# Optimization experiments

Measured on AMD Instinct MI355X. Metric: run time of the kernel, lower is better.

Reference implementation:

```python
import jax, jax.numpy as jnp
import numpy as np

N_BUS = 2048


def setup_inputs() -> dict:
    key = jax.random.key(0)
    ks = jax.random.split(key, 16)
    n_x, n_rbf, n_bus, batch = 4096, 1024, N_BUS, 8192
    s = lambda fan_in: 1.0 / np.sqrt(fan_in)
    return {
        "x": jax.random.normal(ks[0], (batch, n_x), dtype=jnp.float32),
        "W_h": jax.random.uniform(ks[1], (n_rbf, n_x), jnp.float32, -s(n_x), s(n_x)),
        "b_h": jax.random.uniform(ks[2], (n_rbf,), jnp.float32, -s(n_x), s(n_x)),
        "W_h2": jax.random.uniform(ks[3], (n_rbf, n_rbf), jnp.float32, -s(n_rbf), s(n_rbf)),
        "b_h2": jax.random.uniform(ks[4], (n_rbf,), jnp.float32, -s(n_rbf), s(n_rbf)),
        "W_y": jax.random.uniform(ks[5], (2 * n_bus, n_rbf), jnp.float32, -s(n_rbf), s(n_rbf)),
        "b_y": jax.random.uniform(ks[6], (2 * n_bus,), jnp.float32, -s(n_rbf), s(n_rbf)),
        "G": jax.random.uniform(ks[7], (n_bus, n_bus), dtype=jnp.float32),
        "Bm": jax.random.uniform(ks[8], (n_bus, n_bus), dtype=jnp.float32),
        "bias_p": jnp.zeros((1, n_bus), jnp.float32),
        "bias_q": jnp.zeros((1, n_bus), jnp.float32),
        "W_p": jax.random.uniform(ks[9], (n_bus, n_bus), jnp.float32, -s(n_bus), s(n_bus)),
        "b_p": jax.random.uniform(ks[10], (n_bus,), jnp.float32, -s(n_bus), s(n_bus)),
        "W_q": jax.random.uniform(ks[11], (n_bus, n_bus), jnp.float32, -s(n_bus), s(n_bus)),
        "b_q": jax.random.uniform(ks[12], (n_bus,), jnp.float32, -s(n_bus), s(n_bus)),
    }


def reference(x, W_h, b_h, W_h2, b_h2, W_y, b_y, G, Bm, bias_p, bias_q, W_p, b_p, W_q, b_q):
    n_bus = N_BUS
    # encoder (intended math: ReLU activations)
    h1 = jax.nn.relu(x @ W_h.T + b_h)
    h2 = jax.nn.relu(h1 @ W_h2.T + b_h2)
    uw = h2 @ W_y.T + b_y                     # [B, 2*n_bus]
    u, w = uw[:, :n_bus], uw[:, n_bus:]
    # decoder: algebraically identical to summing the masked outer products over dim 2:
    # p_i = sum_k (u_i u_k + w_i w_k) G_ik + (w_i u_k - u_i w_k) B_ik
    #     = u_i (G u)_i + w_i (G w)_i + w_i (B u)_i - u_i (B w)_i
    Gu = u @ G.T
    Gw = w @ G.T
    Bu = u @ Bm.T
    Bw = w @ Bm.T
    p = u * Gu + w * Gw + w * Bu - u * Bw + bias_p
    q = w * Gu - u * Gw - u * Bu - w * Bw + bias_q
    p = p @ W_p.T + b_p
    q = q @ W_q.T + b_q
    return (uw, p, q)
```

## Files before the change

### kernel.cpp

```cpp
#include <hip/hip_runtime.h>
#include <stdint.h>

typedef __bf16 bf16;
typedef __bf16 bf16x8 __attribute__((ext_vector_type(8)));
typedef __bf16 bf16x4 __attribute__((ext_vector_type(4)));
typedef float  f32x4  __attribute__((ext_vector_type(4)));

__device__ __forceinline__ void async_load16(const void* g, void* l) {
    __builtin_amdgcn_global_load_lds(
        (const __attribute__((address_space(1))) void*)g,
        (__attribute__((address_space(3))) void*)l,
        16, 0, 0);
}

__global__ __launch_bounds__(256) void cast_f32_bf16(
        const float* __restrict__ s, bf16* __restrict__ d, int n) {
    int i = (blockIdx.x * 256 + threadIdx.x) * 8;
    if (i >= n) return;
    f32x4 v0 = *(const f32x4*)(s + i);
    f32x4 v1 = *(const f32x4*)(s + i + 4);
    bf16x8 o;
    o[0] = (bf16)v0[0]; o[1] = (bf16)v0[1]; o[2] = (bf16)v0[2]; o[3] = (bf16)v0[3];
    o[4] = (bf16)v1[0]; o[5] = (bf16)v1[1]; o[6] = (bf16)v1[2]; o[7] = (bf16)v1[3];
    *(bf16x8*)(d + i) = o;
}

__global__ __launch_bounds__(256) void fill_f32(float* p, float v, int n) {
    int i = blockIdx.x * 256 + threadIdx.x;
    if (i < n) p[i] = v;
}

template<int RELU, int WF32, int WBF16>
__global__ __launch_bounds__(256, 3) void gemm_bt(
        const bf16* __restrict__ A, int lda,
        const bf16* __restrict__ B, int ldb,
        const float* __restrict__ bias,
        float* __restrict__ Cf, int ldcf,
        bf16* __restrict__ Cb, int ldcb,
        int M, int N, int K) {
    (void)M; (void)N;
    __shared__ __attribute__((aligned(16))) bf16 lA[128 * 32];
    __shared__ __attribute__((aligned(16))) bf16 lB[128 * 32];

    const int t = threadIdx.x;
    const int w = t >> 6, lane = t & 63;
    const int wm = w >> 1, wn = w & 1;
    const int m0 = blockIdx.y * 128, n0 = blockIdx.x * 128;
    const int lane15 = lane & 15, quad = lane >> 4;

    f32x4 acc[4][4] = {};

    const int srow = lane >> 2;
    const int scol = (lane & 3) * 8;
    const int c0 = 2 * w, c1 = 2 * w + 1;
    const bf16* gA0 = A + (size_t)(m0 + c0 * 16 + srow) * lda + scol;
    const bf16* gA1 = A + (size_t)(m0 + c1 * 16 + srow) * lda + scol;
    const bf16* gB0 = B + (size_t)(n0 + c0 * 16 + srow) * ldb + scol;
    const bf16* gB1 = B + (size_t)(n0 + c1 * 16 + srow) * ldb + scol;
    bf16* lA0 = &lA[c0 * 512];
    bf16* lA1 = &lA[c1 * 512];
    bf16* lB0 = &lB[c0 * 512];
    bf16* lB1 = &lB[c1 * 512];

    const bf16* fA = &lA[(wm * 64 + lane15) * 32 + quad * 8];
    const bf16* fB = &lB[(wn * 64 + lane15) * 32 + quad * 8];

    for (int k0 = 0; k0 < K; k0 += 32) {
        async_load16(gA0, lA0);
        async_load16(gA1, lA1);
        async_load16(gB0, lB0);
        async_load16(gB1, lB1);
        gA0 += 32; gA1 += 32; gB0 += 32; gB1 += 32;
        __syncthreads();
        bf16x8 a[4], b[4];
#pragma unroll
        for (int i = 0; i < 4; i++) a[i] = *(const bf16x8*)(fA + i * 16 * 32);
#pragma unroll
        for (int j = 0; j < 4; j++) b[j] = *(const bf16x8*)(fB + j * 16 * 32);
#pragma unroll
        for (int i = 0; i < 4; i++)
#pragma unroll
            for (int j = 0; j < 4; j++)
                acc[i][j] = __builtin_amdgcn_mfma_f32_16x16x32_bf16(a[i], b[j], acc[i][j], 0, 0, 0);
        __syncthreads();
    }

#pragma unroll
    for (int i = 0; i < 4; i++) {
        int row = m0 + wm * 64 + i * 16 + quad * 4;
#pragma unroll
        for (int j = 0; j < 4; j++) {
            int col = n0 + wn * 64 + j * 16 + lane15;
            float bv = bias ? bias[col] : 0.0f;
#pragma unroll
            for (int r = 0; r < 4; r++) {
                float v = acc[i][j][r] + bv;
                if (RELU) v = v > 0.0f ? v : 0.0f;
                if (WF32)  Cf[(size_t)(row + r) * ldcf + col] = v;
                if (WBF16) Cb[(size_t)(row + r) * ldcb + col] = (bf16)v;
            }
        }
    }
}

template<int RELU, int WF32, int WBF16>
__global__ __launch_bounds__(512, 2) void gemm256(
        const bf16* __restrict__ A, int lda,
        const bf16* __restrict__ B, int ldb,
        const float* __restrict__ bias,
        float* __restrict__ Cf, int ldcf,
        bf16* __restrict__ Cb, int ldcb,
        int K) {
    __shared__ __attribute__((aligned(128))) char sm[131072];

    const int t = threadIdx.x;
    const int w = t >> 6;
    const int lane = t & 63;
    const int wm = w >> 2, wn = w & 3;
    const int l15 = lane & 15, quad = lane >> 4;

    const int gx = gridDim.x;
    const int nwg = gx * gridDim.y;
    const int orig = blockIdx.y * gx + blockIdx.x;
    const int cpx = nwg >> 3;
    const int wg = (orig & 7) * cpx + (orig >> 3);
    const int m0 = (wg / gx) << 8;
    const int n0 = (wg % gx) << 8;

    f32x4 acc[8][4] = {};

    const int srow = t >> 3;
    const int scol = ((t & 7) ^ (srow & 7)) << 3;
    const bf16* gA = A + (size_t)(m0 + srow) * lda + scol;
    const bf16* gB = B + (size_t)(n0 + srow) * ldb + scol;
    char* smA = sm + w * 1024;
    char* smB = sm + 65536 + w * 1024;
    const size_t rstepA = (size_t)lda << 6;
    const size_t rstepB = (size_t)ldb << 6;

    const int swz = (quad ^ (l15 & 7)) << 4;
    const char* aRd0 = sm + ((wm * 128 + l15) << 7) + swz;
    const char* bRd0 = sm + 65536 + ((wn * 64 + l15) << 7) + swz;
    const char* aRd1 = (const char*)((uintptr_t)aRd0 ^ 64);
    const char* bRd1 = (const char*)((uintptr_t)bRd0 ^ 64);

    bf16x8 a[4][2], b[4][2];
    unsigned boff = 0;

#define STG_A(c, nb) async_load16(gA + (c) * rstepA, smA + (nb) + (c) * 8192)
#define STG_B(c, nb) async_load16(gB + (c) * rstepB, smB + (nb) + (c) * 8192)
#define RD_A(Mq) do { _Pragma("unroll") \
    for (int i = 0; i < 4; i++) { \
        a[i][0] = *(const bf16x8*)(aRd0 + boff + (Mq) * 8192 + i * 2048); \
        a[i][1] = *(const bf16x8*)(aRd1 + boff + (Mq) * 8192 + i * 2048); } } while (0)
#define RD_B(Nq) do { _Pragma("unroll") \
    for (int j = 0; j < 2; j++) { \
        b[(Nq) * 2 + j][0] = *(const bf16x8*)(bRd0 + boff + ((Nq) * 2 + j) * 2048); \
        b[(Nq) * 2 + j][1] = *(const bf16x8*)(bRd1 + boff + ((Nq) * 2 + j) * 2048); } } while (0)
#define MMA(Mq, Nq) do { _Pragma("unroll") \
    for (int i = 0; i < 4; i++) { _Pragma("unroll") \
        for (int j = 0; j < 2; j++) { \
            acc[(Mq) * 4 + i][(Nq) * 2 + j] = __builtin_amdgcn_mfma_f32_16x16x32_bf16( \
                a[i][0], b[(Nq) * 2 + j][0], acc[(Mq) * 4 + i][(Nq) * 2 + j], 0, 0, 0); \
            acc[(Mq) * 4 + i][(Nq) * 2 + j] = __builtin_amdgcn_mfma_f32_16x16x32_bf16( \
                a[i][1], b[(Nq) * 2 + j][1], acc[(Mq) * 4 + i][(Nq) * 2 + j], 0, 0, 0); } } } while (0)
#define BARP() do { __builtin_amdgcn_s_barrier(); \
    __builtin_amdgcn_sched_barrier(0); } while (0)
#define WAITVM(N) do { \
    asm volatile("s_waitcnt vmcnt(" #N ")" ::: "memory"); } while (0)

    STG_B(0, 0); STG_B(1, 0); STG_B(2, 0); STG_B(3, 0);
    STG_A(0, 0); STG_A(2, 0); STG_A(1, 0); STG_A(3, 0);
    gA += 64; gB += 64;
    WAITVM(0);
    BARP();

    const int nt = K >> 6;
#define KTILE(PF) do { \
    const unsigned nboff = boff ^ 32768u; \
     \
    RD_A(0); RD_B(0); RD_B(1); \
    if (PF) { STG_B(0, nboff); STG_B(1, nboff); STG_B(2, nboff); STG_B(3, nboff); } \
    MMA(0, 0); MMA(0, 1); \
    if (PF) { WAITVM(4); } \
    BARP(); \
     \
    RD_A(1); \
    if (PF) { STG_A(0, nboff); STG_A(2, nboff); STG_A(1, nboff); STG_A(3, nboff); } \
    MMA(1, 0); MMA(1, 1); \
    if (PF) { WAITVM(2); gA += 64; gB += 64; } \
    BARP(); \
    boff = nboff; \
} while (0)

    for (int T = 0; T < nt - 1; ++T) KTILE(1);
    KTILE(0);
#undef KTILE
#undef STG_A
#undef STG_B
#undef RD_A
#undef RD_B
#undef MMA
#undef BARP
#undef WAITVM

#pragma unroll
    for (int i = 0; i < 8; i++) {
        int row = m0 + wm * 128 + i * 16 + quad * 4;
#pragma unroll
        for (int j = 0; j < 4; j++) {
            int col = n0 + wn * 64 + j * 16 + l15;
            float bv = bias ? bias[col] : 0.0f;
#pragma unroll
            for (int r = 0; r < 4; r++) {
                float v = acc[i][j][r] + bv;
                if (RELU) v = v > 0.0f ? v : 0.0f;
                if (WF32)  Cf[(size_t)(row + r) * ldcf + col] = v;
                if (WBF16) Cb[(size_t)(row + r) * ldcb + col] = (bf16)v;
            }
        }
    }
}

__global__ __launch_bounds__(256) void combine_pq(
        const bf16* __restrict__ uwb,
        const bf16* __restrict__ GBu, const bf16* __restrict__ GBw,
        const float* __restrict__ bias_p, const float* __restrict__ bias_q,
        bf16* __restrict__ pp, bf16* __restrict__ qp) {
    int idx = (blockIdx.x * 256 + threadIdx.x) * 4;
    int row = idx >> 11;
    int col = idx & 2047;
    size_t base = (size_t)row * 4096 + col;
    bf16x4 u4  = *(const bf16x4*)(uwb + base);
    bf16x4 w4  = *(const bf16x4*)(uwb + base + 2048);
    bf16x4 gu4 = *(const bf16x4*)(GBu + base);
    bf16x4 bu4 = *(const bf16x4*)(GBu + base + 2048);
    bf16x4 gw4 = *(const bf16x4*)(GBw + base);
    bf16x4 bw4 = *(const bf16x4*)(GBw + base + 2048);
    bf16x4 po, qo;
#pragma unroll
    for (int r = 0; r < 4; r++) {
        float u = (float)u4[r], w = (float)w4[r];
        float gu = (float)gu4[r], gw = (float)gw4[r];
        float bu = (float)bu4[r], bw = (float)bw4[r];
        float p = u * gu + w * gw + w * bu - u * bw + bias_p[col + r];
        float q = w * gu - u * gw - u * bu - w * bw + bias_q[col + r];
        po[r] = (bf16)p;
        qo[r] = (bf16)q;
    }
    *(bf16x4*)(pp + idx) = po;
    *(bf16x4*)(qp + idx) = qo;
}

extern "C" void kernel_launch(void* const* d_in, const int* in_sizes, int n_in,
                              void* d_out, int out_size, void* d_ws, size_t ws_size,
                              hipStream_t stream) {
    (void)in_sizes; (void)n_in;
    const int BT = 8192, NX = 4096, NR = 1024, NB = 2048;

    const float* x      = (const float*)d_in[0];
    const float* W_h    = (const float*)d_in[1];
    const float* b_h    = (const float*)d_in[2];
    const float* W_h2   = (const float*)d_in[3];
    const float* b_h2   = (const float*)d_in[4];
    const float* W_y    = (const float*)d_in[5];
    const float* b_y    = (const float*)d_in[6];
    const float* G      = (const float*)d_in[7];
    const float* Bm     = (const float*)d_in[8];
    const float* bias_p = (const float*)d_in[9];
    const float* bias_q = (const float*)d_in[10];
    const float* W_p    = (const float*)d_in[11];
    const float* b_p    = (const float*)d_in[12];
    const float* W_q    = (const float*)d_in[13];
    const float* b_q    = (const float*)d_in[14];
    float* out = (float*)d_out;

    const size_t NEED = 320864256ull;
    if (ws_size < NEED) {
        fill_f32<<<dim3((out_size + 255) / 256), dim3(256), 0, stream>>>(
            out, (float)(ws_size >> 20), out_size);
        return;
    }
    char* ws = (char*)d_ws;
    bf16* xb   = (bf16*)(ws + 0);
    bf16* GBu  = (bf16*)(ws + 0);
    bf16* uwb  = (bf16*)(ws + 67108864);
    bf16* GBw  = (bf16*)(ws + 134217728);
    bf16* h1   = (bf16*)(ws + 201326592);
    bf16* pp   = (bf16*)(ws + 201326592);
    bf16* h2   = (bf16*)(ws + 218103808);
    bf16* qp   = (bf16*)(ws + 234881024);
    bf16* whb  = (bf16*)(ws + 268435456);
    bf16* wh2b = (bf16*)(ws + 276824064);
    bf16* wyb  = (bf16*)(ws + 278921216);
    bf16* gbm  = (bf16*)(ws + 287309824);
    bf16* wpb  = (bf16*)(ws + 304087040);
    bf16* wqb  = (bf16*)(ws + 312475648);

    dim3 blk(256);
    auto cast = [&](const float* s, bf16* d, int n) {
        cast_f32_bf16<<<dim3((n / 8 + 255) / 256), blk, 0, stream>>>(s, d, n);
    };
    cast(x,    xb,   BT * NX);
    cast(W_h,  whb,  NR * NX);
    cast(W_h2, wh2b, NR * NR);
    cast(W_y,  wyb,  NX * NR);
    cast(G,    gbm,            NB * NB);
    cast(Bm,   gbm + (size_t)NB * NB, NB * NB);
    cast(W_p,  wpb,  NB * NB);
    cast(W_q,  wqb,  NB * NB);

    gemm_bt<1, 0, 1><<<dim3(NR / 128, BT / 128), blk, 0, stream>>>(
        xb, NX, whb, NX, b_h, nullptr, 0, h1, NR, BT, NR, NX);
    gemm_bt<1, 0, 1><<<dim3(NR / 128, BT / 128), blk, 0, stream>>>(
        h1, NR, wh2b, NR, b_h2, nullptr, 0, h2, NR, BT, NR, NR);

    gemm256<0, 1, 1><<<dim3(NX / 256, BT / 256), dim3(512), 0, stream>>>(
        h2, NR, wyb, NR, b_y, out, NX, uwb, NX, NR);
    gemm256<0, 0, 1><<<dim3(NX / 256, BT / 256), dim3(512), 0, stream>>>(
        uwb,      NX, gbm, NB, nullptr, nullptr, 0, GBu, NX, NB);
    gemm256<0, 0, 1><<<dim3(NX / 256, BT / 256), dim3(512), 0, stream>>>(
        uwb + NB, NX, gbm, NB, nullptr, nullptr, 0, GBw, NX, NB);
    combine_pq<<<dim3(BT * NB / 4 / 256), blk, 0, stream>>>(
        uwb, GBu, GBw, bias_p, bias_q, pp, qp);
    gemm256<0, 1, 0><<<dim3(NB / 256, BT / 256), dim3(512), 0, stream>>>(
        pp, NB, wpb, NB, b_p, out + (size_t)BT * NX, NB, nullptr, 0, NB);
    gemm256<0, 1, 0><<<dim3(NB / 256, BT / 256), dim3(512), 0, stream>>>(
        qp, NB, wqb, NB, b_q, out + (size_t)BT * NX + (size_t)BT * NB, NB, nullptr, 0, NB);
}
```

Baseline: 1.277 ms.

## Restructure gemm256 K-loop into finer-grained staged prefetch with setprio and remapped wave tiles

The gemm256 main loop is split into three barrier phases, each issuing part of the next tile's global-to-LDS loads between MFMA groups, with half of the next-next tile prefetched early. MFMA blocks are wrapped in s_setprio to favour math waves. The warp-to-subtile mapping changes so that each wave covers interleaved 64-row and 32-column sub-blocks, with the epilogue indexing adjusted to match. One of the decoder GEMMs is also switched to the 128-tile gemm_bt kernel. The goal is to hide load latency better, at the cost of more barriers and harder-to-verify wait counts.

```diff
diff --git a/kernel.cpp b/kernel.cpp
--- a/kernel.cpp
+++ b/kernel.cpp
@@ -139,62 +139,73 @@
     const size_t rstepB = (size_t)ldb << 6;
 
     const int swz = (quad ^ (l15 & 7)) << 4;
-    const char* aRd0 = sm + ((wm * 128 + l15) << 7) + swz;
-    const char* bRd0 = sm + 65536 + ((wn * 64 + l15) << 7) + swz;
+    const char* aRd0 = sm + (wm << 13) + (l15 << 7) + swz;
+    const char* bRd0 = sm + 65536 + ((wn >> 1) << 13) + ((((wn & 1) << 5) + l15) << 7) + swz;
     const char* aRd1 = (const char*)((uintptr_t)aRd0 ^ 64);
     const char* bRd1 = (const char*)((uintptr_t)bRd0 ^ 64);
 
     bf16x8 a[4][2], b[4][2];
     unsigned boff = 0;
 
-#define STG_A(c, nb) async_load16(gA + (c) * rstepA, smA + (nb) + (c) * 8192)
-#define STG_B(c, nb) async_load16(gB + (c) * rstepB, smB + (nb) + (c) * 8192)
+#define STG_A(c, ko, nb) async_load16(gA + (ko) + (c) * rstepA, smA + (nb) + (c) * 8192)
+#define STG_B(c, ko, nb) async_load16(gB + (ko) + (c) * rstepB, smB + (nb) + (c) * 8192)
 #define RD_A(Mq) do { _Pragma("unroll") \
     for (int i = 0; i < 4; i++) { \
-        a[i][0] = *(const bf16x8*)(aRd0 + boff + (Mq) * 8192 + i * 2048); \
-        a[i][1] = *(const bf16x8*)(aRd1 + boff + (Mq) * 8192 + i * 2048); } } while (0)
+        a[i][0] = *(const bf16x8*)(aRd0 + boff + (Mq) * 16384 + i * 2048); \
+        a[i][1] = *(const bf16x8*)(aRd1 + boff + (Mq) * 16384 + i * 2048); } } while (0)
 #define RD_B(Nq) do { _Pragma("unroll") \
     for (int j = 0; j < 2; j++) { \
-        b[(Nq) * 2 + j][0] = *(const bf16x8*)(bRd0 + boff + ((Nq) * 2 + j) * 2048); \
-        b[(Nq) * 2 + j][1] = *(const bf16x8*)(bRd1 + boff + ((Nq) * 2 + j) * 2048); } } while (0)
-#define MMA(Mq, Nq) do { _Pragma("unroll") \
+        b[(Nq) * 2 + j][0] = *(const bf16x8*)(bRd0 + boff + (Nq) * 16384 + j * 2048); \
+        b[(Nq) * 2 + j][1] = *(const bf16x8*)(bRd1 + boff + (Nq) * 16384 + j * 2048); } } while (0)
+#define MMA(Mq, Nq) do { __builtin_amdgcn_s_setprio(1); _Pragma("unroll") \
     for (int i = 0; i < 4; i++) { _Pragma("unroll") \
         for (int j = 0; j < 2; j++) { \
             acc[(Mq) * 4 + i][(Nq) * 2 + j] = __builtin_amdgcn_mfma_f32_16x16x32_bf16( \
                 a[i][0], b[(Nq) * 2 + j][0], acc[(Mq) * 4 + i][(Nq) * 2 + j], 0, 0, 0); \
             acc[(Mq) * 4 + i][(Nq) * 2 + j] = __builtin_amdgcn_mfma_f32_16x16x32_bf16( \
-                a[i][1], b[(Nq) * 2 + j][1], acc[(Mq) * 4 + i][(Nq) * 2 + j], 0, 0, 0); } } } while (0)
+                a[i][1], b[(Nq) * 2 + j][1], acc[(Mq) * 4 + i][(Nq) * 2 + j], 0, 0, 0); } } \
+    __builtin_amdgcn_s_setprio(0); } while (0)
 #define BARP() do { __builtin_amdgcn_s_barrier(); \
     __builtin_amdgcn_sched_barrier(0); } while (0)
-#define WAITVM(N) do { \
-    asm volatile("s_waitcnt vmcnt(" #N ")" ::: "memory"); } while (0)
-
-    STG_B(0, 0); STG_B(1, 0); STG_B(2, 0); STG_B(3, 0);
-    STG_A(0, 0); STG_A(2, 0); STG_A(1, 0); STG_A(3, 0);
+#define WAITVM_IMPL(N) asm volatile("s_waitcnt vmcnt(" #N ")" ::: "memory")
+#define WAITVM(N) WAITVM_IMPL(N)
+
+    STG_A(0, 0, 0); STG_A(1, 0, 0); STG_B(0, 0, 0); STG_B(1, 0, 0);
+    STG_B(2, 0, 0); STG_B(3, 0, 0); STG_A(2, 0, 0); STG_A(3, 0, 0);
+    STG_A(0, 64, 32768); STG_A(1, 64, 32768); STG_B(0, 64, 32768); STG_B(1, 64, 32768);
     gA += 64; gB += 64;
-    WAITVM(0);
+    WAITVM(8);
     BARP();
 
     const int nt = K >> 6;
-#define KTILE(PF) do { \
+#define KTILE(SG1, SG2, W0, W1, W3) do { \
     const unsigned nboff = boff ^ 32768u; \
      \
-    RD_A(0); RD_B(0); RD_B(1); \
-    if (PF) { STG_B(0, nboff); STG_B(1, nboff); STG_B(2, nboff); STG_B(3, nboff); } \
-    MMA(0, 0); MMA(0, 1); \
-    if (PF) { WAITVM(4); } \
-    BARP(); \
+    RD_A(0); RD_B(0); \
+    if (SG1) { STG_B(2, 0, nboff); STG_B(3, 0, nboff); } \
+    MMA(0, 0); \
+    WAITVM(W0); BARP(); \
+     \
+    RD_B(1); \
+    if (SG1) { STG_A(2, 0, nboff); STG_A(3, 0, nboff); } \
+    MMA(0, 1); \
+    WAITVM(W1); BARP(); \
      \
     RD_A(1); \
-    if (PF) { STG_A(0, nboff); STG_A(2, nboff); STG_A(1, nboff); STG_A(3, nboff); } \
-    MMA(1, 0); MMA(1, 1); \
-    if (PF) { WAITVM(2); gA += 64; gB += 64; } \
-    BARP(); \
+    if (SG2) { STG_A(0, 64, boff); STG_A(1, 64, boff); } \
+    MMA(1, 0); \
+    if (SG2) { STG_B(0, 64, boff); STG_B(1, 64, boff); } \
+    MMA(1, 1); \
+    WAITVM(W3); BARP(); \
     boff = nboff; \
 } while (0)
 
-    for (int T = 0; T < nt - 1; ++T) KTILE(1);
-    KTILE(0);
+    for (int T = 0; T < nt - 2; ++T) {
+        KTILE(1, 1, 8, 8, 8);
+        gA += 64; gB += 64;
+    }
+    KTILE(1, 0, 8, 8, 4);
+    KTILE(0, 0, 2, 0, 0);
 #undef KTILE
 #undef STG_A
 #undef STG_B
@@ -203,13 +214,14 @@
 #undef MMA
 #undef BARP
 #undef WAITVM
+#undef WAITVM_IMPL
 
 #pragma unroll
     for (int i = 0; i < 8; i++) {
-        int row = m0 + wm * 128 + i * 16 + quad * 4;
+        int row = m0 + ((i >> 2) << 7) + (wm << 6) + ((i & 3) << 4) + (quad << 2);
 #pragma unroll
         for (int j = 0; j < 4; j++) {
-            int col = n0 + wn * 64 + j * 16 + l15;
+            int col = n0 + ((j >> 1) << 7) + (wn << 5) + ((j & 1) << 4) + l15;
             float bv = bias ? bias[col] : 0.0f;
 #pragma unroll
             for (int r = 0; r < 4; r++) {
@@ -319,8 +331,8 @@
         h2, NR, wyb, NR, b_y, out, NX, uwb, NX, NR);
     gemm256<0, 0, 1><<<dim3(NX / 256, BT / 256), dim3(512), 0, stream>>>(
         uwb,      NX, gbm, NB, nullptr, nullptr, 0, GBu, NX, NB);
-    gemm256<0, 0, 1><<<dim3(NX / 256, BT / 256), dim3(512), 0, stream>>>(
-        uwb + NB, NX, gbm, NB, nullptr, nullptr, 0, GBw, NX, NB);
+    gemm_bt<0, 0, 1><<<dim3(NX / 128, BT / 128), blk, 0, stream>>>(
+        uwb + NB, NX, gbm, NB, nullptr, nullptr, 0, GBw, NX, BT, NX, NB);
     combine_pq<<<dim3(BT * NB / 4 / 256), blk, 0, stream>>>(
         uwb, GBu, GBw, bias_p, bias_q, pp, qp);
     gemm256<0, 1, 0><<<dim3(NB / 256, BT / 256), dim3(512), 0, stream>>>(
```

Measured after the change: 1.271 ms. Within noise of the previous version (-0.5%).
